# Performance work log

Measured on AMD Instinct MI355X. Metric: run time of the kernel, lower is better.

Reference implementation:

```python
import jax, jax.numpy as jnp
import numpy as np

N_LEAVES = 524288  # layer-0 splats (binary tree)
D_FEAT = 128
NUM_LAYERS = 7          # layers 0..6
ATTN_START = 3          # layers 1,2 -> mean pooling; 3+ -> attention pooling
HOPS = 3                # 2**3 = 8 descendants per ancestor


def setup_inputs() -> dict:
    key = jax.random.key(0)
    k0, k1 = jax.random.split(key)
    x0 = jax.random.normal(k0, (N_LEAVES, D_FEAT), dtype=jnp.float32)
    w_attn = jax.random.normal(k1, (D_FEAT,), dtype=jnp.float32)
    return {"x0": x0, "w_attn": w_attn}


def _mean_pool_pairs(x):
    # x: [P*2, D] -> [P, D]; SplatMeanPooling over 2 children per parent
    P = x.shape[0] // 2
    return jnp.mean(x.reshape(P, 2, x.shape[-1]), axis=1)


def _attn_pool_groups(x, w, k):
    # x: [A*k, D] -> [A, D]; learned-query softmax attention pooling per group
    A, d = x.shape[0] // k, x.shape[-1]
    g = x.reshape(A, k, d)                                  # [A, k, D]
    scale = jnp.asarray(d, g.dtype) ** -0.5
    scores = jnp.einsum('akd,d->ak', g, w) * scale          # [A, k]
    wts = jax.nn.softmax(scores, axis=-1)                   # group softmax
    return jnp.einsum('ak,akd->ad', wts, g)                 # [A, D]


def reference(x0, w_attn):
    # Sequentially build layers 1..NUM_LAYERS-1, mirroring the Python loop:
    #  layer l < ATTN_START : mean over 2 children of layer l-1
    #  layer l >= ATTN_START: attention over 2**HOPS descendants of layer l-HOPS
    layers = [x0]
    for l in range(1, NUM_LAYERS):
        if l < ATTN_START:
            layers.append(_mean_pool_pairs(layers[l - 1]))
        else:
            src = max(0, l - HOPS)
            layers.append(_attn_pool_groups(layers[src], w_attn, 2 ** HOPS))
    # Return all updated layer features (the 'processed tree'), concatenated.
    return jnp.concatenate(layers[1:], axis=0)
```

## Files before the change

### kernel.cpp

```cpp
#include <hip/hip_runtime.h>
#include <math.h>


static constexpr size_t O1 = 0;
static constexpr size_t O2 = 262144ull * 128;
static constexpr size_t O3 = 393216ull * 128;
static constexpr size_t O4 = 458752ull * 128;
static constexpr size_t O5 = 491520ull * 128;
static constexpr size_t O6 = 507904ull * 128;

#define TPB 256

__device__ __forceinline__ float4 f4add(float4 a, float4 b) {
  return make_float4(a.x + b.x, a.y + b.y, a.z + b.z, a.w + b.w);
}
__device__ __forceinline__ float4 f4mul(float4 a, float s) {
  return make_float4(a.x * s, a.y * s, a.z * s, a.w * s);
}
__device__ __forceinline__ float4 f4fma(float4 a, float s, float4 c) {
  return make_float4(fmaf(a.x, s, c.x), fmaf(a.y, s, c.y), fmaf(a.z, s, c.z),
                     fmaf(a.w, s, c.w));
}
__device__ __forceinline__ float f4dot(float4 a, float4 b) {
  return a.x * b.x + a.y * b.y + a.z * b.z + a.w * b.w;
}
__device__ __forceinline__ float slice_sum(float p) {
#pragma unroll
  for (int off = 16; off > 0; off >>= 1) p += __shfl_xor(p, off, 64);
  return p;
}

template <int N>
__device__ __forceinline__ void softmax_n(const float* s, float* wt) {
  float m = s[0];
#pragma unroll
  for (int i = 1; i < N; ++i) m = fmaxf(m, s[i]);
  float sum = 0.f;
#pragma unroll
  for (int i = 0; i < N; ++i) {
    wt[i] = __expf(s[i] - m);
    sum += wt[i];
  }
  const float inv = 1.f / sum;
#pragma unroll
  for (int i = 0; i < N; ++i) wt[i] *= inv;
}

__global__ __launch_bounds__(TPB, 4) void splat_fused(
    const float* __restrict__ x0, const float* __restrict__ w,
    float* __restrict__ out) {
  __shared__ float ssc[24];
  __shared__ float pb5[8][128];
  __shared__ float pb6[8][128];

  const int tid = threadIdx.x;
  const int h = tid >> 5;
  const int cg = tid & 31;
  const int c0 = cg << 2;
  const size_t b = blockIdx.x;
  const float scale = 0.08838834764831845f;

  const float4 wv = *(const float4*)(w + c0);

  float4 xr[8];
  {
    const float* xb = x0 + b * 8192 + (size_t)(h * 8) * 128 + c0;
#pragma unroll
    for (int r = 0; r < 8; ++r) xr[r] = *(const float4*)(xb + r * 128);
  }

  float4 l1[4];
#pragma unroll
  for (int j = 0; j < 4; ++j)
    l1[j] = f4mul(f4add(xr[2 * j], xr[2 * j + 1]), 0.5f);
  {
    float* g = out + O1 + (b * 32 + h * 4) * 128 + c0;
#pragma unroll
    for (int j = 0; j < 4; ++j) *(float4*)(g + j * 128) = l1[j];
  }

  float4 l2[2];
#pragma unroll
  for (int j = 0; j < 2; ++j)
    l2[j] = f4mul(f4add(l1[2 * j], l1[2 * j + 1]), 0.5f);
  {
    float* g = out + O2 + (b * 16 + h * 2) * 128 + c0;
#pragma unroll
    for (int j = 0; j < 2; ++j) *(float4*)(g + j * 128) = l2[j];
  }

  float4 l3;
  {
    float s3[8];
#pragma unroll
    for (int r = 0; r < 8; ++r) s3[r] = slice_sum(f4dot(xr[r], wv)) * scale;
    float wt[8];
    softmax_n<8>(s3, wt);
    l3 = f4mul(xr[0], wt[0]);
#pragma unroll
    for (int r = 1; r < 8; ++r) l3 = f4fma(xr[r], wt[r], l3);
    *(float4*)(out + O3 + (b * 8 + h) * 128 + c0) = l3;
  }

  {
    float s8[8];
#pragma unroll
    for (int j = 0; j < 4; ++j) {
      const float sj = slice_sum(f4dot(l1[j], wv)) * scale;
      const float so = __shfl_xor(sj, 32, 64);
      if (h & 1) {
        s8[j] = so;
        s8[4 + j] = sj;
      } else {
        s8[j] = sj;
        s8[4 + j] = so;
      }
    }
    float wt[8];
    softmax_n<8>(s8, wt);
    const int base = (h & 1) * 4;
    float4 pa = f4mul(l1[0], wt[base]);
#pragma unroll
    for (int j = 1; j < 4; ++j) pa = f4fma(l1[j], wt[base + j], pa);
    pa.x += __shfl_xor(pa.x, 32, 64);
    pa.y += __shfl_xor(pa.y, 32, 64);
    pa.z += __shfl_xor(pa.z, 32, 64);
    pa.w += __shfl_xor(pa.w, 32, 64);
    if (!(h & 1))
      *(float4*)(out + O4 + (b * 4 + (h >> 1)) * 128 + c0) = pa;
  }

  {
#pragma unroll
    for (int j = 0; j < 2; ++j) {
      const float sj = slice_sum(f4dot(l2[j], wv)) * scale;
      if (cg == j) ssc[h * 2 + j] = sj;
    }
    const float s6 = slice_sum(f4dot(l3, wv)) * scale;
    if (cg == 2) ssc[16 + h] = s6;
  }
  __syncthreads();

  {
    float wt5[8];
    softmax_n<8>(ssc + (h >> 2) * 8, wt5);
    const int base = (h & 3) * 2;
    const float4 pa5 = f4fma(l2[1], wt5[base + 1], f4mul(l2[0], wt5[base]));
    *(float4*)(&pb5[h][c0]) = pa5;

    float wt6[8];
    softmax_n<8>(ssc + 16, wt6);
    *(float4*)(&pb6[h][c0]) = f4mul(l3, wt6[h]);
  }
  __syncthreads();

  {
    const int g = tid >> 7, c = tid & 127;
    const float v = pb5[g * 4 + 0][c] + pb5[g * 4 + 1][c] +
                    pb5[g * 4 + 2][c] + pb5[g * 4 + 3][c];
    out[O5 + (b * 2 + g) * 128 + c] = v;
  }
  if (tid < 128) {
    float v = 0.f;
#pragma unroll
    for (int s = 0; s < 8; ++s) v += pb6[s][tid];
    out[O6 + b * 128 + tid] = v;
  }
}

extern "C" void kernel_launch(void* const* d_in, const int* in_sizes, int n_in,
                              void* d_out, int out_size, void* d_ws,
                              size_t ws_size, hipStream_t stream) {
  const float* x0 = (const float*)d_in[0];
  const float* w = (const float*)d_in[1];
  float* out = (float*)d_out;
  const int n_leaves = in_sizes[0] / 128;
  const int blocks = n_leaves / 64;
  splat_fused<<<blocks, TPB, 0, stream>>>(x0, w, out);
}
```

Baseline: 104.2 us.

## Map one wave per row-group with float2 lanes, nontemporal stores, 512-thread blocks

Restructures the fused tree-pooling kernel so each 64-lane wave owns a full 128-wide feature row using float2 per lane, instead of half-waves with float4. Dot products then reduce across the whole wave, and the layer-4 pooling moves into shared memory with the final reductions spread across waves. All output stores become nontemporal. Block size doubles to 512 threads and occupancy hints rise. The aim is fewer cross-half shuffles, better store behaviour for write-once outputs, and more waves in flight, at the cost of narrower loads and extra shared-memory traffic.

```diff
diff --git a/kernel.cpp b/kernel.cpp
--- a/kernel.cpp
+++ b/kernel.cpp
@@ -9,24 +9,24 @@
 static constexpr size_t O5 = 491520ull * 128;
 static constexpr size_t O6 = 507904ull * 128;
 
-#define TPB 256
+#define TPB 512
 
-__device__ __forceinline__ float4 f4add(float4 a, float4 b) {
-  return make_float4(a.x + b.x, a.y + b.y, a.z + b.z, a.w + b.w);
+typedef float f2v __attribute__((ext_vector_type(2)));
+
+__device__ __forceinline__ f2v f2add(f2v a, f2v b) { return a + b; }
+__device__ __forceinline__ f2v f2mul(f2v a, float s) { return a * s; }
+__device__ __forceinline__ f2v f2fma(f2v a, float s, f2v c) {
+  f2v r;
+  r.x = fmaf(a.x, s, c.x);
+  r.y = fmaf(a.y, s, c.y);
+  return r;
 }
-__device__ __forceinline__ float4 f4mul(float4 a, float s) {
-  return make_float4(a.x * s, a.y * s, a.z * s, a.w * s);
+__device__ __forceinline__ void st_nt_f2(float* p, f2v v) {
+  __builtin_nontemporal_store(v, (f2v*)p);
 }
-__device__ __forceinline__ float4 f4fma(float4 a, float s, float4 c) {
-  return make_float4(fmaf(a.x, s, c.x), fmaf(a.y, s, c.y), fmaf(a.z, s, c.z),
-                     fmaf(a.w, s, c.w));
-}
-__device__ __forceinline__ float f4dot(float4 a, float4 b) {
-  return a.x * b.x + a.y * b.y + a.z * b.z + a.w * b.w;
-}
-__device__ __forceinline__ float slice_sum(float p) {
+__device__ __forceinline__ float wave_sum(float p) {
 #pragma unroll
-  for (int off = 16; off > 0; off >>= 1) p += __shfl_xor(p, off, 64);
+  for (int off = 32; off > 0; off >>= 1) p += __shfl_xor(p, off, 64);
   return p;
 }
 
@@ -46,125 +46,117 @@
   for (int i = 0; i < N; ++i) wt[i] *= inv;
 }
 
-__global__ __launch_bounds__(TPB, 4) void splat_fused(
+__global__ __launch_bounds__(TPB, 8) void splat_fused(
     const float* __restrict__ x0, const float* __restrict__ w,
     float* __restrict__ out) {
-  __shared__ float ssc[24];
+  __shared__ float ssc[56];
+  __shared__ float pb4[8][128];
   __shared__ float pb5[8][128];
   __shared__ float pb6[8][128];
 
   const int tid = threadIdx.x;
-  const int h = tid >> 5;
-  const int cg = tid & 31;
-  const int c0 = cg << 2;
+  const int wid = tid >> 6;
+  const int lane = tid & 63;
+  const int c0 = lane << 1;
   const size_t b = blockIdx.x;
   const float scale = 0.08838834764831845f;
 
-  const float4 wv = *(const float4*)(w + c0);
+  f2v qw = *(const f2v*)(w + c0);
 
-  float4 xr[8];
+  f2v xr[8];
   {
-    const float* xb = x0 + b * 8192 + (size_t)(h * 8) * 128 + c0;
+    const float* xb = x0 + b * 8192 + (size_t)(wid * 8) * 128 + c0;
 #pragma unroll
-    for (int r = 0; r < 8; ++r) xr[r] = *(const float4*)(xb + r * 128);
+    for (int r = 0; r < 8; ++r) xr[r] = *(const f2v*)(xb + r * 128);
   }
 
-  float4 l1[4];
-#pragma unroll
-  for (int j = 0; j < 4; ++j)
-    l1[j] = f4mul(f4add(xr[2 * j], xr[2 * j + 1]), 0.5f);
-  {
-    float* g = out + O1 + (b * 32 + h * 4) * 128 + c0;
-#pragma unroll
-    for (int j = 0; j < 4; ++j) *(float4*)(g + j * 128) = l1[j];
-  }
-
-  float4 l2[2];
-#pragma unroll
-  for (int j = 0; j < 2; ++j)
-    l2[j] = f4mul(f4add(l1[2 * j], l1[2 * j + 1]), 0.5f);
-  {
-    float* g = out + O2 + (b * 16 + h * 2) * 128 + c0;
-#pragma unroll
-    for (int j = 0; j < 2; ++j) *(float4*)(g + j * 128) = l2[j];
-  }
-
-  float4 l3;
+  f2v l3;
   {
     float s3[8];
 #pragma unroll
-    for (int r = 0; r < 8; ++r) s3[r] = slice_sum(f4dot(xr[r], wv)) * scale;
+    for (int r = 0; r < 8; ++r)
+      s3[r] = wave_sum(xr[r].x * qw.x + xr[r].y * qw.y) * scale;
     float wt[8];
     softmax_n<8>(s3, wt);
-    l3 = f4mul(xr[0], wt[0]);
+    l3 = f2mul(xr[0], wt[0]);
 #pragma unroll
-    for (int r = 1; r < 8; ++r) l3 = f4fma(xr[r], wt[r], l3);
-    *(float4*)(out + O3 + (b * 8 + h) * 128 + c0) = l3;
+    for (int r = 1; r < 8; ++r) l3 = f2fma(xr[r], wt[r], l3);
+    st_nt_f2(out + O3 + (b * 8 + wid) * 128 + c0, l3);
   }
 
+  f2v l1[4];
+#pragma unroll
+  for (int j = 0; j < 4; ++j)
+    l1[j] = f2mul(f2add(xr[2 * j], xr[2 * j + 1]), 0.5f);
   {
-    float s8[8];
+    float* g = out + O1 + (b * 32 + wid * 4) * 128 + c0;
 #pragma unroll
-    for (int j = 0; j < 4; ++j) {
-      const float sj = slice_sum(f4dot(l1[j], wv)) * scale;
-      const float so = __shfl_xor(sj, 32, 64);
-      if (h & 1) {
-        s8[j] = so;
-        s8[4 + j] = sj;
-      } else {
-        s8[j] = sj;
-        s8[4 + j] = so;
-      }
-    }
-    float wt[8];
-    softmax_n<8>(s8, wt);
-    const int base = (h & 1) * 4;
-    float4 pa = f4mul(l1[0], wt[base]);
+    for (int j = 0; j < 4; ++j) st_nt_f2(g + j * 128, l1[j]);
+  }
+
+  f2v l2[2];
 #pragma unroll
-    for (int j = 1; j < 4; ++j) pa = f4fma(l1[j], wt[base + j], pa);
-    pa.x += __shfl_xor(pa.x, 32, 64);
-    pa.y += __shfl_xor(pa.y, 32, 64);
-    pa.z += __shfl_xor(pa.z, 32, 64);
-    pa.w += __shfl_xor(pa.w, 32, 64);
-    if (!(h & 1))
-      *(float4*)(out + O4 + (b * 4 + (h >> 1)) * 128 + c0) = pa;
+  for (int j = 0; j < 2; ++j)
+    l2[j] = f2mul(f2add(l1[2 * j], l1[2 * j + 1]), 0.5f);
+  {
+    float* g = out + O2 + (b * 16 + wid * 2) * 128 + c0;
+#pragma unroll
+    for (int j = 0; j < 2; ++j) st_nt_f2(g + j * 128, l2[j]);
   }
 
   {
 #pragma unroll
+    for (int j = 0; j < 4; ++j) {
+      const float s4 = wave_sum(l1[j].x * qw.x + l1[j].y * qw.y) * scale;
+      if (lane == 0) ssc[wid * 4 + j] = s4;
+    }
+#pragma unroll
     for (int j = 0; j < 2; ++j) {
-      const float sj = slice_sum(f4dot(l2[j], wv)) * scale;
-      if (cg == j) ssc[h * 2 + j] = sj;
+      const float s5 = wave_sum(l2[j].x * qw.x + l2[j].y * qw.y) * scale;
+      if (lane == 0) ssc[32 + wid * 2 + j] = s5;
     }
-    const float s6 = slice_sum(f4dot(l3, wv)) * scale;
-    if (cg == 2) ssc[16 + h] = s6;
+    const float s6 = wave_sum(l3.x * qw.x + l3.y * qw.y) * scale;
+    if (lane == 0) ssc[48 + wid] = s6;
   }
   __syncthreads();
 
   {
+    float wt4[8];
+    softmax_n<8>(ssc + (wid >> 1) * 8, wt4);
+    const int b4 = (wid & 1) * 4;
+    f2v p4 = f2mul(l1[0], wt4[b4]);
+#pragma unroll
+    for (int j = 1; j < 4; ++j) p4 = f2fma(l1[j], wt4[b4 + j], p4);
+    *(f2v*)(&pb4[wid][c0]) = p4;
+
     float wt5[8];
-    softmax_n<8>(ssc + (h >> 2) * 8, wt5);
-    const int base = (h & 3) * 2;
-    const float4 pa5 = f4fma(l2[1], wt5[base + 1], f4mul(l2[0], wt5[base]));
-    *(float4*)(&pb5[h][c0]) = pa5;
+    softmax_n<8>(ssc + 32 + (wid >> 2) * 8, wt5);
+    const int b5 = (wid & 3) * 2;
+    const f2v p5 = f2fma(l2[1], wt5[b5 + 1], f2mul(l2[0], wt5[b5]));
+    *(f2v*)(&pb5[wid][c0]) = p5;
 
     float wt6[8];
-    softmax_n<8>(ssc + 16, wt6);
-    *(float4*)(&pb6[h][c0]) = f4mul(l3, wt6[h]);
+    softmax_n<8>(ssc + 48, wt6);
+    *(f2v*)(&pb6[wid][c0]) = f2mul(l3, wt6[wid]);
   }
   __syncthreads();
 
-  {
-    const int g = tid >> 7, c = tid & 127;
-    const float v = pb5[g * 4 + 0][c] + pb5[g * 4 + 1][c] +
-                    pb5[g * 4 + 2][c] + pb5[g * 4 + 3][c];
-    out[O5 + (b * 2 + g) * 128 + c] = v;
-  }
-  if (tid < 128) {
-    float v = 0.f;
+  if (wid < 4) {
+    const f2v v = f2add(*(const f2v*)(&pb4[2 * wid][c0]),
+                        *(const f2v*)(&pb4[2 * wid + 1][c0]));
+    st_nt_f2(out + O4 + (b * 4 + wid) * 128 + c0, v);
+  } else if (wid < 6) {
+    const int m = wid - 4;
+    f2v v = f2add(*(const f2v*)(&pb5[4 * m][c0]),
+                  *(const f2v*)(&pb5[4 * m + 1][c0]));
+    v = f2add(v, *(const f2v*)(&pb5[4 * m + 2][c0]));
+    v = f2add(v, *(const f2v*)(&pb5[4 * m + 3][c0]));
+    st_nt_f2(out + O5 + (b * 2 + m) * 128 + c0, v);
+  } else if (wid == 6) {
+    f2v v = *(const f2v*)(&pb6[0][c0]);
 #pragma unroll
-    for (int s = 0; s < 8; ++s) v += pb6[s][tid];
-    out[O6 + b * 128 + tid] = v;
+    for (int s = 1; s < 8; ++s) v = f2add(v, *(const f2v*)(&pb6[s][c0]));
+    st_nt_f2(out + O6 + b * 128 + c0, v);
   }
 }
 
```

Result: slower. 109.5 us (+5.1%).
